# Kernel tuning notes

Measured on AMD Instinct MI355X. Metric: run time of the kernel, lower is better.

Reference implementation:

```python
import jax, jax.numpy as jnp
import numpy as np

N = 50000      # nodes
E = 500000     # edges (avg degree 10)
IN = 256       # in_feats
HID = 64       # hid_feats (per-head out dim)
H = 4          # num_heads


def setup_inputs() -> dict:
    key = jax.random.key(0)
    ks = jax.random.split(key, 16)
    f32 = jnp.float32
    def rn(k, shape, s=0.05):
        return jax.random.normal(k, shape, dtype=f32) * s
    return {
        "x": jax.random.normal(ks[0], (N, IN), dtype=f32),
        "src": jax.random.randint(ks[1], (E,), 0, N, dtype=jnp.int32),
        "dst": jax.random.randint(ks[2], (E,), 0, N, dtype=jnp.int32),
        "embed_W": rn(ks[3], (IN, HID)), "embed_b": jnp.zeros((HID,), f32),
        "W1": rn(ks[4], (HID, H * HID)),
        "al1": rn(ks[5], (H, HID)), "ar1": rn(ks[6], (H, HID)),
        "b1": jnp.zeros((H * HID,), f32),
        "W2": rn(ks[7], (H * HID, H * HID)),
        "al2": rn(ks[8], (H, HID)), "ar2": rn(ks[9], (H, HID)),
        "b2": jnp.zeros((H * HID,), f32),
        "p1_W": rn(ks[10], (H * HID, HID)), "p1_b": jnp.zeros((HID,), f32),
        "p2_W": rn(ks[11], (HID, 1)), "p2_b": jnp.zeros((1,), f32),
    }


def _gat_conv(x, W, al, ar, b, src, dst):
    """DGL GATConv: linear proj, per-edge LeakyReLU attention, edge softmax over dst, scatter-sum."""
    feat = (x @ W).reshape(N, H, HID)                    # [N,H,F]
    el = jnp.einsum('nhf,hf->nh', feat, al)              # [N,H]
    er = jnp.einsum('nhf,hf->nh', feat, ar)              # [N,H]
    e = jax.nn.leaky_relu(el[src] + er[dst], 0.2)        # [E,H]
    m = jax.ops.segment_max(e, dst, num_segments=N)      # per-dst max (stable softmax)
    ex = jnp.exp(e - m[dst])                             # [E,H]
    s = jax.ops.segment_sum(ex, dst, num_segments=N)     # [N,H]
    alpha = ex / s[dst]                                  # edge softmax weights
    out = jax.ops.segment_sum(alpha[:, :, None] * feat[src], dst, num_segments=N)  # [N,H,F]
    return out + b.reshape(1, H, HID)


def reference(x, src, dst, embed_W, embed_b, W1, al1, ar1, b1,
              W2, al2, ar2, b2, p1_W, p1_b, p2_W, p2_b):
    h = x @ embed_W + embed_b                                        # embed: [N,HID]
    h = jax.nn.relu(_gat_conv(h, W1, al1, ar1, b1, src, dst))        # [N,H,HID]
    h = h.reshape(N, H * HID)
    h = jax.nn.relu(_gat_conv(h, W2, al2, ar2, b2, src, dst))        # [N,H,HID]
    h = h.reshape(N, H * HID)
    return jax.nn.sigmoid((h @ p1_W + p1_b) @ p2_W + p2_b)           # [N,1]
```

## Files before the change

### kernel.cpp

```cpp
#include <hip/hip_runtime.h>
#include <hip/hip_bf16.h>

#define NN 50000
#define NE 500000
#define C_HH 256

typedef __attribute__((ext_vector_type(8))) short s16x8;
typedef __attribute__((ext_vector_type(4))) float f32x4;
typedef __attribute__((ext_vector_type(4))) unsigned short u16x4;
typedef unsigned short ushort_t;

__device__ __forceinline__ float lrelu(float x) { return x > 0.f ? x : 0.2f * x; }

__device__ __forceinline__ ushort_t f2bf(float f) {
  unsigned u = __float_as_uint(f);
  u = (u + 0x7FFFu + ((u >> 16) & 1u)) >> 16;
  return (ushort_t)u;
}
__device__ __forceinline__ float bf2f(ushort_t u) {
  return __uint_as_float(((unsigned)u) << 16);
}
__device__ __forceinline__ float sel_head(float4 v, int head) {
  const float x0 = (head & 1) ? v.y : v.x;
  const float x1 = (head & 1) ? v.w : v.z;
  return (head & 2) ? x1 : x0;
}

__global__ __launch_bounds__(256) void prep_kernel(const float* __restrict__ eW,
                                                   const float* __restrict__ W1,
                                                   const float* __restrict__ eb,
                                                   const float* __restrict__ W2,
                                                   const float* __restrict__ p1W,
                                                   const float* __restrict__ p1b,
                                                   const float* __restrict__ p2W,
                                                   const float* __restrict__ p2b,
                                                   ushort_t* __restrict__ WcT,
                                                   ushort_t* __restrict__ w2T,
                                                   float* __restrict__ bc,
                                                   float* __restrict__ qv,
                                                   float* __restrict__ cv) {
  int idx = blockIdx.x * 256 + threadIdx.x;
  if (idx < 65536) {
    const int n = idx >> 8, k = idx & 255;
    float s = 0.f;
#pragma unroll 8
    for (int j = 0; j < 64; ++j) s = fmaf(eW[k * 64 + j], W1[j * 256 + n], s);
    WcT[idx] = f2bf(s);
  } else if (idx < 131072) {
    idx -= 65536;
    const int n = idx >> 8, k = idx & 255;
    w2T[idx] = f2bf(W2[k * 256 + n]);
  } else if (idx < 131328) {
    const int n = idx - 131072;
    float s = 0.f;
#pragma unroll 8
    for (int j = 0; j < 64; ++j) s = fmaf(eb[j], W1[j * 256 + n], s);
    bc[n] = s;
  } else if (idx < 131584) {
    const int k = idx - 131328;
    float s = 0.f;
#pragma unroll 8
    for (int j = 0; j < 64; ++j) s = fmaf(p1W[k * 64 + j], p2W[j], s);
    qv[k] = s;
  } else if (idx == 131584) {
    float s = p2b[0];
    for (int j = 0; j < 64; ++j) s = fmaf(p1b[j], p2W[j], s);
    cv[0] = s;
  }
}

template <bool A_F32, bool BIAS>
__global__ __launch_bounds__(256, 2) void gemm_fused(const void* __restrict__ Ain,
                                                     const ushort_t* __restrict__ WT,
                                                     const float* __restrict__ bc,
                                                     const float* __restrict__ al,
                                                     const float* __restrict__ ar,
                                                     float* __restrict__ el,
                                                     float* __restrict__ er,
                                                     ushort_t* __restrict__ Cout, int M) {
  const int wid = threadIdx.x >> 6;
  const int lane = threadIdx.x & 63;
  const int row0 = blockIdx.x * 32;
  const int rA = lane & 15;
  const int kg = lane >> 4;
  const int c0 = wid * 64;

  const s16x8 zf = {0, 0, 0, 0, 0, 0, 0, 0};
  const bool v0 = (row0 + rA) < M;
  const bool v1 = (row0 + 16 + rA) < M;
  const ushort_t* Wbase = WT + (size_t)(c0 + rA) * 256;

  s16x8 a0[8], a1[8];
  if (A_F32) {
    const float* Af = (const float*)Ain;
    const float* Ar0 = Af + (size_t)(row0 + rA) * 256;
    const float* Ar1 = Af + (size_t)(row0 + 16 + rA) * 256;
    const f32x4 zf4 = {0.f, 0.f, 0.f, 0.f};
    f32x4 af0[8][2], af1[8][2];
#pragma unroll
    for (int ks = 0; ks < 8; ++ks) {
      const int k0 = ks * 32 + kg * 8;
      af0[ks][0] = v0 ? *reinterpret_cast<const f32x4*>(Ar0 + k0) : zf4;
      af0[ks][1] = v0 ? *reinterpret_cast<const f32x4*>(Ar0 + k0 + 4) : zf4;
      af1[ks][0] = v1 ? *reinterpret_cast<const f32x4*>(Ar1 + k0) : zf4;
      af1[ks][1] = v1 ? *reinterpret_cast<const f32x4*>(Ar1 + k0 + 4) : zf4;
    }
#pragma unroll
    for (int ks = 0; ks < 8; ++ks) {
#pragma unroll
      for (int h = 0; h < 2; ++h) {
#pragma unroll
        for (int j = 0; j < 4; ++j) {
          a0[ks][h * 4 + j] = (short)f2bf(af0[ks][h][j]);
          a1[ks][h * 4 + j] = (short)f2bf(af1[ks][h][j]);
        }
      }
    }
  } else {
    const ushort_t* Ab = (const ushort_t*)Ain;
    const ushort_t* Ar0 = Ab + (size_t)(row0 + rA) * 256;
    const ushort_t* Ar1 = Ab + (size_t)(row0 + 16 + rA) * 256;
#pragma unroll
    for (int ks = 0; ks < 8; ++ks) {
      const int k0 = ks * 32 + kg * 8;
      a0[ks] = v0 ? *reinterpret_cast<const s16x8*>(Ar0 + k0) : zf;
      a1[ks] = v1 ? *reinterpret_cast<const s16x8*>(Ar1 + k0) : zf;
    }
  }

  s16x8 b[8][4];
#pragma unroll
  for (int ks = 0; ks < 8; ++ks) {
    const int k0 = ks * 32 + kg * 8;
#pragma unroll
    for (int nt = 0; nt < 4; ++nt)
      b[ks][nt] = *reinterpret_cast<const s16x8*>(Wbase + nt * 16 * 256 + k0);
  }

  f32x4 acc[2][4] = {};
#pragma unroll
  for (int ks = 0; ks < 8; ++ks) {
#pragma unroll
    for (int nt = 0; nt < 4; ++nt) {
      acc[0][nt] = __builtin_amdgcn_mfma_f32_16x16x32_bf16(a0[ks], b[ks][nt], acc[0][nt], 0, 0, 0);
      acc[1][nt] = __builtin_amdgcn_mfma_f32_16x16x32_bf16(a1[ks], b[ks][nt], acc[1][nt], 0, 0, 0);
    }
  }

  if (BIAS) {
#pragma unroll
    for (int nt = 0; nt < 4; ++nt) {
      const float bv = bc[c0 + nt * 16 + rA];
#pragma unroll
      for (int mt = 0; mt < 2; ++mt)
#pragma unroll
        for (int i = 0; i < 4; ++i) acc[mt][nt][i] += bv;
    }
  }

#pragma unroll
  for (int nt = 0; nt < 4; ++nt) {
    const int col = c0 + nt * 16 + rA;
#pragma unroll
    for (int mt = 0; mt < 2; ++mt) {
#pragma unroll
      for (int i = 0; i < 4; ++i) {
        const int row = row0 + mt * 16 + kg * 4 + i;
        if (row < M) Cout[(size_t)row * 256 + col] = f2bf(acc[mt][nt][i]);
      }
    }
  }

  float alv[4], arv[4];
#pragma unroll
  for (int nt = 0; nt < 4; ++nt) {
    alv[nt] = al[c0 + nt * 16 + rA];
    arv[nt] = ar[c0 + nt * 16 + rA];
  }
#pragma unroll
  for (int mt = 0; mt < 2; ++mt) {
#pragma unroll
    for (int i = 0; i < 4; ++i) {
      float e = 0.f, r = 0.f;
#pragma unroll
      for (int nt = 0; nt < 4; ++nt) {
        e = fmaf(acc[mt][nt][i], alv[nt], e);
        r = fmaf(acc[mt][nt][i], arv[nt], r);
      }
#pragma unroll
      for (int m = 1; m < 16; m <<= 1) {
        e += __shfl_xor(e, m);
        r += __shfl_xor(r, m);
      }
      const int row = row0 + mt * 16 + kg * 4 + i;
      if (rA == 0 && row < M) {
        el[row * 4 + wid] = e;
        er[row * 4 + wid] = r;
      }
    }
  }
}

__global__ __launch_bounds__(256) void hist_kernel(const int* __restrict__ dst,
                                                   int* __restrict__ rowptr) {
  const int e = blockIdx.x * 256 + threadIdx.x;
  if (e < NE) atomicAdd(&rowptr[dst[e]], 1);
}

__global__ __launch_bounds__(256) void scan1_kernel(int* __restrict__ rowptr,
                                                    int* __restrict__ partial) {
  __shared__ int sh[256];
  const int t = threadIdx.x;
  const int i = blockIdx.x * 256 + t;
  const int v = (i < NN) ? rowptr[i] : 0;
  sh[t] = v;
  __syncthreads();
#pragma unroll
  for (int off = 1; off < 256; off <<= 1) {
    int x = (t >= off) ? sh[t - off] : 0;
    __syncthreads();
    sh[t] += x;
    __syncthreads();
  }
  if (i < NN) rowptr[i] = sh[t] - v;
  if (t == 255) partial[blockIdx.x] = sh[255];
}

__global__ __launch_bounds__(256) void scan2_kernel(int* __restrict__ partial, int npb) {
  __shared__ int sh[256];
  const int t = threadIdx.x;
  const int v = (t < npb) ? partial[t] : 0;
  sh[t] = v;
  __syncthreads();
#pragma unroll
  for (int off = 1; off < 256; off <<= 1) {
    int x = (t >= off) ? sh[t - off] : 0;
    __syncthreads();
    sh[t] += x;
    __syncthreads();
  }
  if (t < npb) partial[t] = sh[t] - v;
}

__global__ __launch_bounds__(256) void scan3_kernel(int* __restrict__ rowptr,
                                                    const int* __restrict__ partial,
                                                    int* __restrict__ cursor) {
  const int i = blockIdx.x * 256 + threadIdx.x;
  if (i < NN) {
    const int r = rowptr[i] + partial[i >> 8];
    rowptr[i] = r;
    cursor[i] = r;
  } else if (i == NN) {
    rowptr[NN] = NE;
  }
}

__global__ __launch_bounds__(256) void scatter_kernel(const int* __restrict__ src,
                                                      const int* __restrict__ dst,
                                                      int* __restrict__ cursor,
                                                      int* __restrict__ sorted_src) {
  const int e = blockIdx.x * 256 + threadIdx.x;
  if (e >= NE) return;
  const int pos = atomicAdd(&cursor[dst[e]], 1);
  sorted_src[pos] = src[e];
}

#define EDGE_BODY(SN, AV, FV)                                    \
  {                                                              \
    const float w_ = __expf(lrelu(sel_head(AV, head) + erh));    \
    a0 = fmaf(w_, bf2f(FV[0]), a0);                              \
    a1 = fmaf(w_, bf2f(FV[1]), a1);                              \
    a2 = fmaf(w_, bf2f(FV[2]), a2);                              \
    a3 = fmaf(w_, bf2f(FV[3]), a3);                              \
    s += w_;                                                     \
  }

template <bool HEAD>
__global__ __launch_bounds__(256) void aggr_fused_kernel(const int* __restrict__ rowptr,
                                                         const int* __restrict__ sorted_src,
                                                         const float* __restrict__ el,
                                                         const float* __restrict__ er,
                                                         const ushort_t* __restrict__ featb,
                                                         const float* __restrict__ bias,
                                                         ushort_t* __restrict__ out,
                                                         const float* __restrict__ qv,
                                                         const float* __restrict__ cv,
                                                         float* __restrict__ outf) {
  const int node = blockIdx.x * 4 + (threadIdx.x >> 6);
  const int lane = threadIdx.x & 63;
  const int head = lane >> 4;
  const int start = rowptr[node];
  const int end = rowptr[node + 1];
  const float erh = sel_head(*reinterpret_cast<const float4*>(er + node * 4), head);
  const size_t lofs = (size_t)lane * 4;

  float a0 = 0.f, a1 = 0.f, a2 = 0.f, a3 = 0.f, s = 0.f;
  int e = start;
  for (; e + 8 <= end; e += 8) {
    const int sn0 = sorted_src[e + 0];
    const int sn1 = sorted_src[e + 1];
    const int sn2 = sorted_src[e + 2];
    const int sn3 = sorted_src[e + 3];
    const int sn4 = sorted_src[e + 4];
    const int sn5 = sorted_src[e + 5];
    const int sn6 = sorted_src[e + 6];
    const int sn7 = sorted_src[e + 7];
    const float4 A0 = *reinterpret_cast<const float4*>(el + sn0 * 4);
    const float4 A1 = *reinterpret_cast<const float4*>(el + sn1 * 4);
    const float4 A2 = *reinterpret_cast<const float4*>(el + sn2 * 4);
    const float4 A3 = *reinterpret_cast<const float4*>(el + sn3 * 4);
    const float4 A4 = *reinterpret_cast<const float4*>(el + sn4 * 4);
    const float4 A5 = *reinterpret_cast<const float4*>(el + sn5 * 4);
    const float4 A6 = *reinterpret_cast<const float4*>(el + sn6 * 4);
    const float4 A7 = *reinterpret_cast<const float4*>(el + sn7 * 4);
    const u16x4 F0 = *reinterpret_cast<const u16x4*>(featb + (size_t)sn0 * C_HH + lofs);
    const u16x4 F1 = *reinterpret_cast<const u16x4*>(featb + (size_t)sn1 * C_HH + lofs);
    const u16x4 F2 = *reinterpret_cast<const u16x4*>(featb + (size_t)sn2 * C_HH + lofs);
    const u16x4 F3 = *reinterpret_cast<const u16x4*>(featb + (size_t)sn3 * C_HH + lofs);
    const u16x4 F4 = *reinterpret_cast<const u16x4*>(featb + (size_t)sn4 * C_HH + lofs);
    const u16x4 F5 = *reinterpret_cast<const u16x4*>(featb + (size_t)sn5 * C_HH + lofs);
    const u16x4 F6 = *reinterpret_cast<const u16x4*>(featb + (size_t)sn6 * C_HH + lofs);
    const u16x4 F7 = *reinterpret_cast<const u16x4*>(featb + (size_t)sn7 * C_HH + lofs);
    EDGE_BODY(sn0, A0, F0) EDGE_BODY(sn1, A1, F1)
    EDGE_BODY(sn2, A2, F2) EDGE_BODY(sn3, A3, F3)
    EDGE_BODY(sn4, A4, F4) EDGE_BODY(sn5, A5, F5)
    EDGE_BODY(sn6, A6, F6) EDGE_BODY(sn7, A7, F7)
  }
  if (e + 4 <= end) {
    const int sn0 = sorted_src[e + 0];
    const int sn1 = sorted_src[e + 1];
    const int sn2 = sorted_src[e + 2];
    const int sn3 = sorted_src[e + 3];
    const float4 A0 = *reinterpret_cast<const float4*>(el + sn0 * 4);
    const float4 A1 = *reinterpret_cast<const float4*>(el + sn1 * 4);
    const float4 A2 = *reinterpret_cast<const float4*>(el + sn2 * 4);
    const float4 A3 = *reinterpret_cast<const float4*>(el + sn3 * 4);
    const u16x4 F0 = *reinterpret_cast<const u16x4*>(featb + (size_t)sn0 * C_HH + lofs);
    const u16x4 F1 = *reinterpret_cast<const u16x4*>(featb + (size_t)sn1 * C_HH + lofs);
    const u16x4 F2 = *reinterpret_cast<const u16x4*>(featb + (size_t)sn2 * C_HH + lofs);
    const u16x4 F3 = *reinterpret_cast<const u16x4*>(featb + (size_t)sn3 * C_HH + lofs);
    EDGE_BODY(sn0, A0, F0) EDGE_BODY(sn1, A1, F1)
    EDGE_BODY(sn2, A2, F2) EDGE_BODY(sn3, A3, F3)
    e += 4;
  }
  for (; e < end; ++e) {
    const int sn = sorted_src[e];
    const float4 A = *reinterpret_cast<const float4*>(el + sn * 4);
    const u16x4 F = *reinterpret_cast<const u16x4*>(featb + (size_t)sn * C_HH + lofs);
    EDGE_BODY(sn, A, F)
  }

  float r0 = 0.f, r1 = 0.f, r2 = 0.f, r3 = 0.f;
  if (end > start) {
    const float inv = 1.f / s;
    r0 = a0 * inv; r1 = a1 * inv; r2 = a2 * inv; r3 = a3 * inv;
  }
  const float4 bb = *reinterpret_cast<const float4*>(bias + lane * 4);
  r0 = fmaxf(r0 + bb.x, 0.f);
  r1 = fmaxf(r1 + bb.y, 0.f);
  r2 = fmaxf(r2 + bb.z, 0.f);
  r3 = fmaxf(r3 + bb.w, 0.f);

  if (!HEAD) {
    u16x4 o;
    o[0] = f2bf(r0); o[1] = f2bf(r1); o[2] = f2bf(r2); o[3] = f2bf(r3);
    *reinterpret_cast<u16x4*>(out + (size_t)node * C_HH + lofs) = o;
  } else {
    const float4 q = *reinterpret_cast<const float4*>(qv + lane * 4);
    float v = fmaf(r0, q.x, fmaf(r1, q.y, fmaf(r2, q.z, r3 * q.w)));
#pragma unroll
    for (int off = 32; off; off >>= 1) v += __shfl_xor(v, off);
    if (lane == 0) outf[node] = 1.f / (1.f + __expf(-(v + cv[0])));
  }
}

extern "C" void kernel_launch(void* const* d_in, const int* in_sizes, int n_in,
                              void* d_out, int out_size, void* d_ws, size_t ws_size,
                              hipStream_t stream) {
  const float* x = (const float*)d_in[0];
  const int* src = (const int*)d_in[1];
  const int* dst = (const int*)d_in[2];
  const float* embed_W = (const float*)d_in[3];
  const float* embed_b = (const float*)d_in[4];
  const float* W1 = (const float*)d_in[5];
  const float* al1 = (const float*)d_in[6];
  const float* ar1 = (const float*)d_in[7];
  const float* b1 = (const float*)d_in[8];
  const float* W2 = (const float*)d_in[9];
  const float* al2 = (const float*)d_in[10];
  const float* ar2 = (const float*)d_in[11];
  const float* b2 = (const float*)d_in[12];
  const float* p1_W = (const float*)d_in[13];
  const float* p1_b = (const float*)d_in[14];
  const float* p2_W = (const float*)d_in[15];
  const float* p2_b = (const float*)d_in[16];

  char* ws = (char*)d_ws;
  ushort_t* featb = (ushort_t*)(ws + 0);
  ushort_t* houtb = (ushort_t*)(ws + 25600000);
  float* el = (float*)(ws + 51200000);
  float* er = (float*)(ws + 52000000);
  int* rowptr = (int*)(ws + 52800000);
  int* cursor = (int*)(ws + 53100000);
  int* partial = (int*)(ws + 53400000);
  int* sorted_src = (int*)(ws + 53500000);
  ushort_t* WcT = (ushort_t*)(ws + 55600000);
  ushort_t* w2T = (ushort_t*)(ws + 55800000);
  float* bc = (float*)(ws + 56000000);
  float* qv = (float*)(ws + 56010000);
  float* cv = (float*)(ws + 56020000);

  const int gEdge = (NE + 255) / 256;
  const int nScanB = (NN + 255) / 256;
  const int gGemm = (NN + 31) / 32;
  const int gNode = NN / 4;

  hipMemsetAsync(rowptr, 0, (NN + 1) * sizeof(int), stream);
  hist_kernel<<<gEdge, 256, 0, stream>>>(dst, rowptr);
  scan1_kernel<<<nScanB, 256, 0, stream>>>(rowptr, partial);
  scan2_kernel<<<1, 256, 0, stream>>>(partial, nScanB);
  scan3_kernel<<<nScanB + 1, 256, 0, stream>>>(rowptr, partial, cursor);
  scatter_kernel<<<gEdge, 256, 0, stream>>>(src, dst, cursor, sorted_src);

  prep_kernel<<<515, 256, 0, stream>>>(embed_W, W1, embed_b, W2, p1_W, p1_b, p2_W, p2_b,
                                       WcT, w2T, bc, qv, cv);

  gemm_fused<true, true><<<gGemm, 256, 0, stream>>>(x, WcT, bc, al1, ar1, el, er, featb, NN);
  aggr_fused_kernel<false><<<gNode, 256, 0, stream>>>(rowptr, sorted_src, el, er, featb, b1,
                                                      houtb, nullptr, nullptr, nullptr);

  gemm_fused<false, false><<<gGemm, 256, 0, stream>>>(houtb, w2T, nullptr, al2, ar2, el, er,
                                                      featb, NN);
  aggr_fused_kernel<true><<<gNode, 256, 0, stream>>>(rowptr, sorted_src, el, er, featb, b2,
                                                     nullptr, qv, cv, (float*)d_out);
}
```

Measured before the change: 389.3 us.

## Pre-swizzle weights into MFMA fragment order and pre-convert x to bf16

The prep kernel now writes the transposed bf16 weights in MFMA fragment order, so each lane loads its B fragment with one contiguous 16-byte read inside the k-loop instead of holding all weight fragments in registers. A new kernel converts x to bf16 ahead of time, and the GEMM is reduced to 16 rows per block with the bounds checks removed, giving more blocks and lower register pressure. The cost is an extra pass that reads x and writes a 25.6MB bf16 copy, and the weights are now re-read from L2 by every block. Because the bounds checks are gone, the GEMM relies on NN being divisible by 16.

After: 356.8 us. -8.3%, faster.

```diff
diff --git a/kernel.cpp b/kernel.cpp
--- a/kernel.cpp
+++ b/kernel.cpp
@@ -24,6 +24,21 @@
   const float x0 = (head & 1) ? v.y : v.x;
   const float x1 = (head & 1) ? v.w : v.z;
   return (head & 2) ? x1 : x0;
+}
+
+__global__ __launch_bounds__(256) void xb_kernel(const float* __restrict__ in,
+                                                 ushort_t* __restrict__ out) {
+  const int n8 = NN * 256 / 8;
+  for (int i = blockIdx.x * 256 + threadIdx.x; i < n8; i += gridDim.x * 256) {
+    const f32x4 v0 = reinterpret_cast<const f32x4*>(in)[2 * i];
+    const f32x4 v1 = reinterpret_cast<const f32x4*>(in)[2 * i + 1];
+    s16x8 o;
+    o[0] = (short)f2bf(v0[0]); o[1] = (short)f2bf(v0[1]);
+    o[2] = (short)f2bf(v0[2]); o[3] = (short)f2bf(v0[3]);
+    o[4] = (short)f2bf(v1[0]); o[5] = (short)f2bf(v1[1]);
+    o[6] = (short)f2bf(v1[2]); o[7] = (short)f2bf(v1[3]);
+    reinterpret_cast<s16x8*>(out)[i] = o;
+  }
 }
 
 __global__ __launch_bounds__(256) void prep_kernel(const float* __restrict__ eW,
@@ -41,15 +56,25 @@
                                                    float* __restrict__ cv) {
   int idx = blockIdx.x * 256 + threadIdx.x;
   if (idx < 65536) {
-    const int n = idx >> 8, k = idx & 255;
+    const int j = idx & 7;
+    const int lane = (idx >> 3) & 63;
+    const int ks = (idx >> 9) & 7;
+    const int gnt = (idx >> 12) & 15;
+    const int k = ks * 32 + (lane >> 4) * 8 + j;
+    const int n = gnt * 16 + (lane & 15);
     float s = 0.f;
 #pragma unroll 8
-    for (int j = 0; j < 64; ++j) s = fmaf(eW[k * 64 + j], W1[j * 256 + n], s);
+    for (int jj = 0; jj < 64; ++jj) s = fmaf(eW[k * 64 + jj], W1[jj * 256 + n], s);
     WcT[idx] = f2bf(s);
   } else if (idx < 131072) {
-    idx -= 65536;
-    const int n = idx >> 8, k = idx & 255;
-    w2T[idx] = f2bf(W2[k * 256 + n]);
+    const int t = idx - 65536;
+    const int j = t & 7;
+    const int lane = (t >> 3) & 63;
+    const int ks = (t >> 9) & 7;
+    const int gnt = (t >> 12) & 15;
+    const int k = ks * 32 + (lane >> 4) * 8 + j;
+    const int n = gnt * 16 + (lane & 15);
+    w2T[t] = f2bf(W2[k * 256 + n]);
   } else if (idx < 131328) {
     const int n = idx - 131072;
     float s = 0.f;
@@ -69,81 +94,35 @@
   }
 }
 
-template <bool A_F32, bool BIAS>
-__global__ __launch_bounds__(256, 2) void gemm_fused(const void* __restrict__ Ain,
-                                                     const ushort_t* __restrict__ WT,
-                                                     const float* __restrict__ bc,
-                                                     const float* __restrict__ al,
-                                                     const float* __restrict__ ar,
-                                                     float* __restrict__ el,
-                                                     float* __restrict__ er,
-                                                     ushort_t* __restrict__ Cout, int M) {
+template <bool BIAS>
+__global__ __launch_bounds__(256) void gemm_fused(const ushort_t* __restrict__ A,
+                                                  const ushort_t* __restrict__ WT,
+                                                  const float* __restrict__ bc,
+                                                  const float* __restrict__ al,
+                                                  const float* __restrict__ ar,
+                                                  float* __restrict__ el,
+                                                  float* __restrict__ er,
+                                                  ushort_t* __restrict__ Cout) {
   const int wid = threadIdx.x >> 6;
   const int lane = threadIdx.x & 63;
-  const int row0 = blockIdx.x * 32;
+  const int row0 = blockIdx.x * 16;
   const int rA = lane & 15;
   const int kg = lane >> 4;
   const int c0 = wid * 64;
 
-  const s16x8 zf = {0, 0, 0, 0, 0, 0, 0, 0};
-  const bool v0 = (row0 + rA) < M;
-  const bool v1 = (row0 + 16 + rA) < M;
-  const ushort_t* Wbase = WT + (size_t)(c0 + rA) * 256;
-
-  s16x8 a0[8], a1[8];
-  if (A_F32) {
-    const float* Af = (const float*)Ain;
-    const float* Ar0 = Af + (size_t)(row0 + rA) * 256;
-    const float* Ar1 = Af + (size_t)(row0 + 16 + rA) * 256;
-    const f32x4 zf4 = {0.f, 0.f, 0.f, 0.f};
-    f32x4 af0[8][2], af1[8][2];
-#pragma unroll
-    for (int ks = 0; ks < 8; ++ks) {
-      const int k0 = ks * 32 + kg * 8;
-      af0[ks][0] = v0 ? *reinterpret_cast<const f32x4*>(Ar0 + k0) : zf4;
-      af0[ks][1] = v0 ? *reinterpret_cast<const f32x4*>(Ar0 + k0 + 4) : zf4;
-      af1[ks][0] = v1 ? *reinterpret_cast<const f32x4*>(Ar1 + k0) : zf4;
-      af1[ks][1] = v1 ? *reinterpret_cast<const f32x4*>(Ar1 + k0 + 4) : zf4;
-    }
-#pragma unroll
-    for (int ks = 0; ks < 8; ++ks) {
-#pragma unroll
-      for (int h = 0; h < 2; ++h) {
-#pragma unroll
-        for (int j = 0; j < 4; ++j) {
-          a0[ks][h * 4 + j] = (short)f2bf(af0[ks][h][j]);
-          a1[ks][h * 4 + j] = (short)f2bf(af1[ks][h][j]);
-        }
-      }
-    }
-  } else {
-    const ushort_t* Ab = (const ushort_t*)Ain;
-    const ushort_t* Ar0 = Ab + (size_t)(row0 + rA) * 256;
-    const ushort_t* Ar1 = Ab + (size_t)(row0 + 16 + rA) * 256;
-#pragma unroll
-    for (int ks = 0; ks < 8; ++ks) {
-      const int k0 = ks * 32 + kg * 8;
-      a0[ks] = v0 ? *reinterpret_cast<const s16x8*>(Ar0 + k0) : zf;
-      a1[ks] = v1 ? *reinterpret_cast<const s16x8*>(Ar1 + k0) : zf;
-    }
-  }
-
-  s16x8 b[8][4];
+  const ushort_t* Arow = A + (size_t)(row0 + rA) * 256 + kg * 8;
+  s16x8 a[8];
+#pragma unroll
+  for (int ks = 0; ks < 8; ++ks) a[ks] = *reinterpret_cast<const s16x8*>(Arow + ks * 32);
+
+  f32x4 acc[4] = {};
 #pragma unroll
   for (int ks = 0; ks < 8; ++ks) {
-    const int k0 = ks * 32 + kg * 8;
-#pragma unroll
-    for (int nt = 0; nt < 4; ++nt)
-      b[ks][nt] = *reinterpret_cast<const s16x8*>(Wbase + nt * 16 * 256 + k0);
-  }
-
-  f32x4 acc[2][4] = {};
-#pragma unroll
-  for (int ks = 0; ks < 8; ++ks) {
 #pragma unroll
     for (int nt = 0; nt < 4; ++nt) {
-      acc[0][nt] = __builtin_amdgcn_mfma_f32_16x16x32_bf16(a0[ks], b[ks][nt], acc[0][nt], 0, 0, 0);
-      acc[1][nt] = __builtin_amdgcn_mfma_f32_16x16x32_bf16(a1[ks], b[ks][nt], acc[1][nt], 0, 0, 0);
+      const s16x8 b = *reinterpret_cast<const s16x8*>(
+          WT + ((size_t)((wid * 4 + nt) * 8 + ks)) * 512 + lane * 8);
+      acc[nt] = __builtin_amdgcn_mfma_f32_16x16x32_bf16(a[ks], b, acc[nt], 0, 0, 0);
     }
   }
 
@@ -152,9 +131,7 @@
     for (int nt = 0; nt < 4; ++nt) {
       const float bv = bc[c0 + nt * 16 + rA];
 #pragma unroll
-      for (int mt = 0; mt < 2; ++mt)
-#pragma unroll
-        for (int i = 0; i < 4; ++i) acc[mt][nt][i] += bv;
+      for (int i = 0; i < 4; ++i) acc[nt][i] += bv;
     }
   }
 
@@ -162,12 +139,9 @@
   for (int nt = 0; nt < 4; ++nt) {
     const int col = c0 + nt * 16 + rA;
 #pragma unroll
-    for (int mt = 0; mt < 2; ++mt) {
-#pragma unroll
-      for (int i = 0; i < 4; ++i) {
-        const int row = row0 + mt * 16 + kg * 4 + i;
-        if (row < M) Cout[(size_t)row * 256 + col] = f2bf(acc[mt][nt][i]);
-      }
+    for (int i = 0; i < 4; ++i) {
+      const int row = row0 + kg * 4 + i;
+      Cout[(size_t)row * 256 + col] = f2bf(acc[nt][i]);
     }
   }
 
@@ -178,25 +152,22 @@
     arv[nt] = ar[c0 + nt * 16 + rA];
   }
 #pragma unroll
-  for (int mt = 0; mt < 2; ++mt) {
-#pragma unroll
-    for (int i = 0; i < 4; ++i) {
-      float e = 0.f, r = 0.f;
-#pragma unroll
-      for (int nt = 0; nt < 4; ++nt) {
-        e = fmaf(acc[mt][nt][i], alv[nt], e);
-        r = fmaf(acc[mt][nt][i], arv[nt], r);
-      }
-#pragma unroll
-      for (int m = 1; m < 16; m <<= 1) {
-        e += __shfl_xor(e, m);
-        r += __shfl_xor(r, m);
-      }
-      const int row = row0 + mt * 16 + kg * 4 + i;
-      if (rA == 0 && row < M) {
-        el[row * 4 + wid] = e;
-        er[row * 4 + wid] = r;
-      }
+  for (int i = 0; i < 4; ++i) {
+    float e = 0.f, r = 0.f;
+#pragma unroll
+    for (int nt = 0; nt < 4; ++nt) {
+      e = fmaf(acc[nt][i], alv[nt], e);
+      r = fmaf(acc[nt][i], arv[nt], r);
+    }
+#pragma unroll
+    for (int m = 1; m < 16; m <<= 1) {
+      e += __shfl_xor(e, m);
+      r += __shfl_xor(r, m);
+    }
+    const int row = row0 + kg * 4 + i;
+    if (rA == 0) {
+      el[row * 4 + wid] = e;
+      er[row * 4 + wid] = r;
     }
   }
 }
@@ -398,21 +369,22 @@
   char* ws = (char*)d_ws;
   ushort_t* featb = (ushort_t*)(ws + 0);
   ushort_t* houtb = (ushort_t*)(ws + 25600000);
-  float* el = (float*)(ws + 51200000);
-  float* er = (float*)(ws + 52000000);
-  int* rowptr = (int*)(ws + 52800000);
-  int* cursor = (int*)(ws + 53100000);
-  int* partial = (int*)(ws + 53400000);
-  int* sorted_src = (int*)(ws + 53500000);
-  ushort_t* WcT = (ushort_t*)(ws + 55600000);
-  ushort_t* w2T = (ushort_t*)(ws + 55800000);
-  float* bc = (float*)(ws + 56000000);
-  float* qv = (float*)(ws + 56010000);
-  float* cv = (float*)(ws + 56020000);
+  ushort_t* xb = (ushort_t*)(ws + 51200000);
+  float* el = (float*)(ws + 76800000);
+  float* er = (float*)(ws + 77600000);
+  int* rowptr = (int*)(ws + 78400000);
+  int* cursor = (int*)(ws + 78700000);
+  int* partial = (int*)(ws + 79000000);
+  int* sorted_src = (int*)(ws + 79100000);
+  ushort_t* WcT = (ushort_t*)(ws + 81200000);
+  ushort_t* w2T = (ushort_t*)(ws + 81400000);
+  float* bc = (float*)(ws + 81600000);
+  float* qv = (float*)(ws + 81610000);
+  float* cv = (float*)(ws + 81620000);
 
   const int gEdge = (NE + 255) / 256;
   const int nScanB = (NN + 255) / 256;
-  const int gGemm = (NN + 31) / 32;
+  const int gGemm = NN / 16;
   const int gNode = NN / 4;
 
   hipMemsetAsync(rowptr, 0, (NN + 1) * sizeof(int), stream);
@@ -424,13 +396,13 @@
 
   prep_kernel<<<515, 256, 0, stream>>>(embed_W, W1, embed_b, W2, p1_W, p1_b, p2_W, p2_b,
                                        WcT, w2T, bc, qv, cv);
-
-  gemm_fused<true, true><<<gGemm, 256, 0, stream>>>(x, WcT, bc, al1, ar1, el, er, featb, NN);
+  xb_kernel<<<2048, 256, 0, stream>>>(x, xb);
+
+  gemm_fused<true><<<gGemm, 256, 0, stream>>>(xb, WcT, bc, al1, ar1, el, er, featb);
   aggr_fused_kernel<false><<<gNode, 256, 0, stream>>>(rowptr, sorted_src, el, er, featb, b1,
                                                       houtb, nullptr, nullptr, nullptr);
 
-  gemm_fused<false, false><<<gGemm, 256, 0, stream>>>(houtb, w2T, nullptr, al2, ar2, el, er,
-                                                      featb, NN);
+  gemm_fused<false><<<gGemm, 256, 0, stream>>>(houtb, w2T, nullptr, al2, ar2, el, er, featb);
   aggr_fused_kernel<true><<<gNode, 256, 0, stream>>>(rowptr, sorted_src, el, er, featb, b2,
                                                      nullptr, qv, cv, (float*)d_out);
 }
```
